# Optimization experiments

Hardware: AMD Instinct MI355X
Metric: run time of the kernel (lower is better)

The kernel has to match this reference:

```python
import jax, jax.numpy as jnp
import numpy as np

G = 8            # grid_size
G2 = G * G       # total_grid_size = 64
NS = 2.0         # neighborhood_size
H = 64           # h_dim
A = 1024         # bottleneck_dim == attention_dim
S = 32           # number of sequences
N = 64           # pedestrians per sequence
P = 4096         # scene boundary points per sequence (down_samples)
B = S * N        # total batch = 2048


def setup_inputs() -> dict:
    key = jax.random.key(0)
    ks = jax.random.split(key, 16)
    starts = jnp.arange(S, dtype=jnp.int32) * N
    seq_start_end = jnp.stack([starts, starts + N], axis=1)  # (S, 2) uniform groups
    return {
        "h_states": jax.random.normal(ks[0], (1, B, H), jnp.float32),
        "end_pos": jax.random.normal(ks[1], (B, 2), jnp.float32),
        "rel_pos": jax.random.normal(ks[2], (B, 2), jnp.float32) * 0.1,
        "scene_info": jax.random.normal(ks[3], (S, P, 2), jnp.float32),
        # Attention_Decoder params (soft attention over G2 grid cells, encoder_dim=1)
        "W_enc": jax.random.normal(ks[4], (1, A), jnp.float32) * 0.05,
        "b_enc": jnp.zeros((A,), jnp.float32),
        "W_dec": jax.random.normal(ks[5], (H, A), jnp.float32) * 0.05,
        "b_dec": jnp.zeros((A,), jnp.float32),
        "w_full": jax.random.normal(ks[6], (A, 1), jnp.float32) * 0.05,
        "b_full": jnp.zeros((1,), jnp.float32),
        "W_out": jax.random.normal(ks[7], (1 + H + 4, A), jnp.float32) * 0.05,  # [ctx, h, embed_info]
        "b_out": jnp.zeros((A,), jnp.float32),
        # mlp_pool: Linear(A, A) + BatchNorm1d + ReLU
        "W_mlp": jax.random.normal(ks[8], (A, A), jnp.float32) * 0.05,
        "b_mlp": jnp.zeros((A,), jnp.float32),
        "gamma": jnp.ones((A,), jnp.float32),
        "beta": jnp.zeros((A,), jnp.float32),
        "seq_start_end": seq_start_end,
    }


def _occupancy(end_pos, scene_info, num_seqs, peds, grid_size, ns):
    """Vectorized per-pedestrian grid-cell binning + scatter-add occupancy.
    end_pos: (num_seqs*peds, 2), scene_info: (num_seqs, P, 2) -> (B, G2)."""
    g2 = grid_size * grid_size
    b = num_seqs * peds
    ep = end_pos.reshape(num_seqs, peds, 1, 2)
    sx = scene_info[:, None, :, 0]  # (S, 1, P)
    sy = scene_info[:, None, :, 1]
    tl_x = ep[..., 0] - ns / 2
    tl_y = ep[..., 1] + ns / 2
    br_x = ep[..., 0] + ns / 2
    br_y = ep[..., 1] - ns / 2
    cell_x = jnp.floor((sx - tl_x) / ns * grid_size)   # (S, N, P)
    cell_y = jnp.floor((tl_y - sy) / ns * grid_size)
    cell = (cell_x + cell_y * grid_size).astype(jnp.int32)
    # point is out-of-bound if outside the ped's neighborhood box (matches torch mask)
    oob = (sx >= br_x) | (sx <= tl_x) | (sy >= tl_y) | (sy <= br_y)
    ped = jnp.arange(b, dtype=jnp.int32).reshape(num_seqs, peds, 1)
    # torch scatters masked points into slot 0 then drops it; we use one dump slot at the end
    idx = jnp.where(oob, b * g2, ped * g2 + cell)      # (S, N, P)
    counts = jax.ops.segment_sum(
        jnp.ones(idx.size, jnp.float32), idx.reshape(-1), num_segments=b * g2 + 1)
    return counts[:-1].reshape(b, g2)


def reference(h_states, end_pos, rel_pos, scene_info,
              W_enc, b_enc, W_dec, b_dec, w_full, b_full,
              W_out, b_out, W_mlp, b_mlp, gamma, beta, seq_start_end):
    num_seqs = seq_start_end.shape[0]
    b = end_pos.shape[0]
    peds = b // num_seqs
    occ = _occupancy(end_pos, scene_info, num_seqs, peds, G, NS)   # (B, G2)
    enc = occ[..., None]                                           # (B, G2, 1)
    h = h_states.reshape(b, -1)                                    # (B, H)
    embed_info = jnp.concatenate([end_pos, rel_pos], axis=1)       # (B, 4)
    # soft attention over the G2 grid cells conditioned on the decoder hidden state
    att = jax.nn.relu(enc @ W_enc + b_enc + (h @ W_dec + b_dec)[:, None, :])  # (B, G2, A)
    e = (att @ w_full)[..., 0] + b_full                            # (B, G2)
    alpha = jax.nn.softmax(e, axis=1)
    ctx = jnp.sum(alpha[..., None] * enc, axis=1)                  # (B, 1)
    pool = jnp.concatenate([ctx, h, embed_info], axis=1) @ W_out + b_out  # (B, A)
    # mlp_pool: Linear -> BatchNorm1d (training stats, biased var) -> ReLU
    y = pool @ W_mlp + b_mlp
    mu = jnp.mean(y, axis=0)
    var = jnp.mean((y - mu) ** 2, axis=0)
    y = gamma * (y - mu) * jax.lax.rsqrt(var + 1e-5) + beta
    return jax.nn.relu(y)
```

## Files before the change

kernel.cpp:

```cpp
#include <hip/hip_runtime.h>
#include <hip/hip_bf16.h>


#define NG2  64
#define NPTS 4096

typedef unsigned short ushort_t;
typedef __attribute__((ext_vector_type(8))) short bf16x8;
typedef __attribute__((ext_vector_type(4))) float f32x4;

struct PrepPtrs { const void* p[16]; };

__device__ __forceinline__ float bf2f(ushort_t u) {
  return __uint_as_float(((unsigned int)u) << 16);
}
__device__ __forceinline__ ushort_t f2bf(float f) {
  __hip_bfloat16 b = __float2bfloat16(f);
  return *reinterpret_cast<ushort_t*>(&b);
}
__device__ __forceinline__ float lde(const void* p, size_t i, int fl) {
  return fl ? bf2f(((const ushort_t*)p)[i]) : ((const float*)p)[i];
}
__device__ __forceinline__ int block_flag(const ushort_t* h) {
  __shared__ int bad_sh;
  if (threadIdx.x == 0) bad_sh = 0;
  __syncthreads();
  float v = bf2f(h[threadIdx.x & 255]);
  if (!(fabsf(v) <= 1e4f)) atomicOr(&bad_sh, 1);
  __syncthreads();
  return (bad_sh == 0) ? 1 : 0;
}

__device__ __forceinline__ void tp_body(const void* in, int fl, int job,
                                        int Kin, int Kpad, ushort_t* out) {
  __shared__ ushort_t t[32][40];
  int n0 = (job & 31) * 32, k0 = (job >> 5) * 32;
  int r = threadIdx.x >> 3, c4 = (threadIdx.x & 7) * 4;
  ushort4 v = make_ushort4(0, 0, 0, 0);
  if (k0 + r < Kin) {
    size_t off = (size_t)(k0 + r) * 1024 + n0 + c4;
    if (fl) {
      v = *(const ushort4*)((const ushort_t*)in + off);
    } else {
      float4 f = *(const float4*)((const float*)in + off);
      v = make_ushort4(f2bf(f.x), f2bf(f.y), f2bf(f.z), f2bf(f.w));
    }
  }
  *(ushort4*)(&t[r][c4]) = v;
  __syncthreads();
  int n = threadIdx.x >> 3, kk = (threadIdx.x & 7) * 4;
  ushort4 o = make_ushort4(t[kk][n], t[kk + 1][n], t[kk + 2][n], t[kk + 3][n]);
  *(ushort4*)(out + (size_t)(n0 + n) * Kpad + k0 + kk) = o;
}

__global__ __launch_bounds__(256) void k_prep(PrepPtrs ptrs,
                                              float* __restrict__ conv,
                                              ushort_t* __restrict__ hbf,
                                              ushort_t* __restrict__ WdecT,
                                              ushort_t* __restrict__ WoutT,
                                              ushort_t* __restrict__ WmlpT,
                                              ushort_t* __restrict__ Xcat0,
                                              float* __restrict__ occ,
                                              float* __restrict__ stats) {
  int b = blockIdx.x;
  int fl = block_flag((const ushort_t*)ptrs.p[0]);
  if (b < 9) {
    int idx = (b * 256 + threadIdx.x) * 4;
    int seg = idx >> 10, off = idx & 1023;
    float4 o;
    if (fl) {
      const unsigned int* src = (const unsigned int*)ptrs.p[7 + seg];
      uint2 u = *(const uint2*)(src + (off >> 1));
      o.x = __uint_as_float((u.x & 0xFFFFu) << 16);
      o.y = __uint_as_float(u.x & 0xFFFF0000u);
      o.z = __uint_as_float((u.y & 0xFFFFu) << 16);
      o.w = __uint_as_float(u.y & 0xFFFF0000u);
    } else {
      o = *(const float4*)((const float*)ptrs.p[7 + seg] + off);
    }
    *(float4*)(conv + idx) = o;
  } else if (b < 73) {
    int i = (b - 9) * 256 + threadIdx.x;
    if (fl) {
      ((uint4*)hbf)[i] = ((const uint4*)ptrs.p[0])[i];
    } else {
      float4 f0 = ((const float4*)ptrs.p[0])[2 * i];
      float4 f1 = ((const float4*)ptrs.p[0])[2 * i + 1];
      ((ushort4*)hbf)[2 * i]     = make_ushort4(f2bf(f0.x), f2bf(f0.y), f2bf(f0.z), f2bf(f0.w));
      ((ushort4*)hbf)[2 * i + 1] = make_ushort4(f2bf(f1.x), f2bf(f1.y), f2bf(f1.z), f2bf(f1.w));
    }
  } else if (b < 137) {
    tp_body(ptrs.p[1], fl, b - 73, 64, 64, WdecT);
  } else if (b < 233) {
    const void* wout1 = fl ? (const void*)((const ushort_t*)ptrs.p[2] + 1024)
                           : (const void*)((const float*)ptrs.p[2] + 1024);
    tp_body(wout1, fl, b - 137, 68, 96, WoutT);
  } else if (b < 489) {
    __shared__ ushort_t t64[64 * 68];
    int job = b - 233;
    int n0 = (job & 15) * 64, k0 = (job >> 4) * 64;
    const void* in = ptrs.p[3];
#pragma unroll
    for (int i = 0; i < 4; i++) {
      int chunk = threadIdx.x + i * 256;
      int r = chunk >> 4, c4 = (chunk & 15) * 4;
      ushort4 v;
      size_t off = (size_t)(k0 + r) * 1024 + n0 + c4;
      if (fl) {
        v = *(const ushort4*)((const ushort_t*)in + off);
      } else {
        float4 f = *(const float4*)((const float*)in + off);
        v = make_ushort4(f2bf(f.x), f2bf(f.y), f2bf(f.z), f2bf(f.w));
      }
      *(ushort4*)(&t64[r * 68 + c4]) = v;
    }
    __syncthreads();
#pragma unroll
    for (int i = 0; i < 4; i++) {
      int chunk = threadIdx.x + i * 256;
      int n = chunk >> 4, k4 = (chunk & 15) * 4;
      ushort4 o = make_ushort4(t64[(k4 + 0) * 68 + n], t64[(k4 + 1) * 68 + n],
                               t64[(k4 + 2) * 68 + n], t64[(k4 + 3) * 68 + n]);
      *(ushort4*)(WmlpT + (size_t)(n0 + n) * 1024 + k0 + k4) = o;
    }
  } else if (b < 681) {
    int flat = (b - 489) * 256 + threadIdx.x;
    int e4 = flat * 4;
    int r = e4 / 96, c = e4 - r * 96;
    ushort4 v = make_ushort4(0, 0, 0, 0);
    if (c < 64) {
      if (fl) v = *(const ushort4*)((const ushort_t*)ptrs.p[0] + r * 64 + c);
      else {
        float4 f = *(const float4*)((const float*)ptrs.p[0] + r * 64 + c);
        v = make_ushort4(f2bf(f.x), f2bf(f.y), f2bf(f.z), f2bf(f.w));
      }
    } else if (c == 64) {
      v.x = f2bf(lde(ptrs.p[4], 2 * r, fl));
      v.y = f2bf(lde(ptrs.p[4], 2 * r + 1, fl));
      v.z = f2bf(lde(ptrs.p[5], 2 * r, fl));
      v.w = f2bf(lde(ptrs.p[5], 2 * r + 1, fl));
    }
    *(ushort4*)(Xcat0 + e4) = v;
  } else if (b < 2729) {
    int i = b - 681;
    int s = i >> 6;
    __shared__ float cnth[NG2];
    if (threadIdx.x < NG2) cnth[threadIdx.x] = 0.0f;
    __syncthreads();
    float ex = lde(ptrs.p[4], 2 * i, fl), ey = lde(ptrs.p[4], 2 * i + 1, fl);
    float tlx = ex - 1.0f, tly = ey + 1.0f, brx = ex + 1.0f, bry = ey - 1.0f;
    const void* scn = ptrs.p[6];
    for (int p = threadIdx.x; p < NPTS; p += 256) {
      size_t pi = (size_t)s * NPTS + p;
      float sx, sy;
      if (fl) {
        unsigned int u = ((const unsigned int*)scn)[pi];
        sx = __uint_as_float((u & 0xFFFFu) << 16);
        sy = __uint_as_float(u & 0xFFFF0000u);
      } else {
        float2 f = *((const float2*)scn + pi);
        sx = f.x; sy = f.y;
      }
      bool oob = (sx >= brx) || (sx <= tlx) || (sy >= tly) || (sy <= bry);
      if (!oob) {
        int cx = (int)floorf((sx - tlx) * 0.5f * 8.0f);
        int cy = (int)floorf((tly - sy) * 0.5f * 8.0f);
        int cell = cx + cy * 8;
        if (cell >= 0 && cell < NG2) atomicAdd(&cnth[cell], 1.0f);
      }
    }
    __syncthreads();
    if (threadIdx.x < NG2) occ[i * NG2 + threadIdx.x] = cnth[threadIdx.x];
  } else {
#pragma unroll
    for (int k = 0; k < 8; k++) stats[threadIdx.x + 256 * k] = 0.0f;
  }
}

template <int K, int EPI>
__device__ __forceinline__ void mgemm_body(
    ushort_t* As, ushort_t* Bs, int m0, int n0,
    const ushort_t* __restrict__ A, int lda,
    const ushort_t* __restrict__ BT, int ldb,
    const float* __restrict__ bias1, const float* __restrict__ bias2,
    ushort_t* __restrict__ outb, float* __restrict__ outf) {
  int tid = threadIdx.x;
  int wave = tid >> 6, lane = tid & 63, l15 = lane & 15, kg = lane >> 4;
  f32x4 acc[4][2] = {};
  int ar = tid >> 2, ag = tid & 3;
  int aswz = ag ^ ((ar >> 1) & 3);
  for (int k0 = 0; k0 < K; k0 += 32) {
    uint4 av = *(const uint4*)(A + (size_t)(m0 + ar) * lda + k0 + ag * 8);
    *(uint4*)(&As[ar * 32 + aswz * 8]) = av;
#pragma unroll
    for (int i = 0; i < 2; i++) {
      int c = tid + i * 256;
      int br = c >> 2, bg = c & 3;
      int bswz = bg ^ ((br >> 1) & 3);
      uint4 bv = *(const uint4*)(BT + (size_t)(n0 + br) * ldb + k0 + bg * 8);
      *(uint4*)(&Bs[br * 32 + bswz * 8]) = bv;
    }
    __syncthreads();
    bf16x8 af[4], bfr[2];
#pragma unroll
    for (int mt = 0; mt < 4; mt++) {
      int row = mt * 16 + l15;
      int swz = kg ^ ((row >> 1) & 3);
      af[mt] = *(const bf16x8*)(&As[row * 32 + swz * 8]);
    }
#pragma unroll
    for (int nt = 0; nt < 2; nt++) {
      int row = wave * 32 + nt * 16 + l15;
      int swz = kg ^ ((row >> 1) & 3);
      bfr[nt] = *(const bf16x8*)(&Bs[row * 32 + swz * 8]);
    }
#pragma unroll
    for (int mt = 0; mt < 4; mt++)
#pragma unroll
      for (int nt = 0; nt < 2; nt++)
        acc[mt][nt] = __builtin_amdgcn_mfma_f32_16x16x32_bf16(af[mt], bfr[nt], acc[mt][nt], 0, 0, 0);
    __syncthreads();
  }
#pragma unroll
  for (int nt = 0; nt < 2; nt++) {
    int col = n0 + wave * 32 + nt * 16 + l15;
    float bsum = (EPI == 0) ? (bias1[col] + bias2[col]) : bias1[col];
#pragma unroll
    for (int mt = 0; mt < 4; mt++) {
#pragma unroll
      for (int r = 0; r < 4; r++) {
        int rowm = m0 + mt * 16 + kg * 4 + r;
        float v = acc[mt][nt][r] + bsum;
        if (EPI == 3) outf[(size_t)rowm * 1024 + col] = v;
        else outb[(size_t)rowm * 1024 + col] = f2bf(v);
      }
    }
  }
}

__global__ __launch_bounds__(256) void k_gemm2(
    const ushort_t* __restrict__ hbf, const ushort_t* __restrict__ WdecT,
    const float* __restrict__ benc, const float* __restrict__ bdec,
    ushort_t* __restrict__ hd_out,
    const ushort_t* __restrict__ Xcat0, const ushort_t* __restrict__ WoutT,
    const float* __restrict__ bout, float* __restrict__ P1) {
  __shared__ ushort_t As[64 * 32];
  __shared__ ushort_t Bs[128 * 32];
  int m0 = blockIdx.x * 64, n0 = blockIdx.y * 128;
  if (blockIdx.z == 0)
    mgemm_body<64, 0>(As, Bs, m0, n0, hbf, 64, WdecT, 64, benc, bdec, hd_out, nullptr);
  else
    mgemm_body<96, 3>(As, Bs, m0, n0, Xcat0, 96, WoutT, 96, bout, nullptr, nullptr, P1);
}

__global__ __launch_bounds__(256) void k_ygemm(
    const ushort_t* __restrict__ A, const ushort_t* __restrict__ BT,
    const float* __restrict__ bias1, ushort_t* __restrict__ outb,
    float* __restrict__ stats) {
  __shared__ ushort_t As[64 * 32];
  __shared__ ushort_t Bs[128 * 32];
  int m0 = blockIdx.x * 64, n0 = blockIdx.y * 128;
  int tid = threadIdx.x;
  int wave = tid >> 6, lane = tid & 63, l15 = lane & 15, kg = lane >> 4;
  f32x4 acc[4][2] = {};
  int ar = tid >> 2, ag = tid & 3;
  int aswz = ag ^ ((ar >> 1) & 3);
  for (int k0 = 0; k0 < 1024; k0 += 32) {
    uint4 av = *(const uint4*)(A + (size_t)(m0 + ar) * 1024 + k0 + ag * 8);
    *(uint4*)(&As[ar * 32 + aswz * 8]) = av;
#pragma unroll
    for (int i = 0; i < 2; i++) {
      int c = tid + i * 256;
      int br = c >> 2, bg = c & 3;
      int bswz = bg ^ ((br >> 1) & 3);
      uint4 bv = *(const uint4*)(BT + (size_t)(n0 + br) * 1024 + k0 + bg * 8);
      *(uint4*)(&Bs[br * 32 + bswz * 8]) = bv;
    }
    __syncthreads();
    bf16x8 af[4], bfr[2];
#pragma unroll
    for (int mt = 0; mt < 4; mt++) {
      int row = mt * 16 + l15;
      int swz = kg ^ ((row >> 1) & 3);
      af[mt] = *(const bf16x8*)(&As[row * 32 + swz * 8]);
    }
#pragma unroll
    for (int nt = 0; nt < 2; nt++) {
      int row = wave * 32 + nt * 16 + l15;
      int swz = kg ^ ((row >> 1) & 3);
      bfr[nt] = *(const bf16x8*)(&Bs[row * 32 + swz * 8]);
    }
#pragma unroll
    for (int mt = 0; mt < 4; mt++)
#pragma unroll
      for (int nt = 0; nt < 2; nt++)
        acc[mt][nt] = __builtin_amdgcn_mfma_f32_16x16x32_bf16(af[mt], bfr[nt], acc[mt][nt], 0, 0, 0);
    __syncthreads();
  }
#pragma unroll
  for (int nt = 0; nt < 2; nt++) {
    int col = n0 + wave * 32 + nt * 16 + l15;
    float bsum = bias1[col];
    float s1 = 0.0f, s2 = 0.0f;
#pragma unroll
    for (int mt = 0; mt < 4; mt++) {
#pragma unroll
      for (int r = 0; r < 4; r++) {
        int rowm = m0 + mt * 16 + kg * 4 + r;
        float v = acc[mt][nt][r] + bsum;
        outb[(size_t)rowm * 1024 + col] = f2bf(v);
        s1 += v; s2 = fmaf(v, v, s2);
      }
    }
    s1 += __shfl_down(s1, 16); s2 += __shfl_down(s2, 16);
    s1 += __shfl_down(s1, 32); s2 += __shfl_down(s2, 32);
    if (lane < 16) {
      atomicAdd(&stats[col], s1);
      atomicAdd(&stats[1024 + col], s2);
    }
  }
}

__global__ __launch_bounds__(256) void k_ectx(
    const float* __restrict__ occ,
    const float* __restrict__ Wenc, const float* __restrict__ wfull,
    const float* __restrict__ w0, const float* __restrict__ P1,
    const ushort_t* __restrict__ hd, ushort_t* __restrict__ pool) {
  __shared__ float we_sh[1024];
  __shared__ float wf_sh[1024];
  __shared__ float hd_sh[4][1024];
  __shared__ float occ_sh[4][64];
  int wave = threadIdx.x >> 6, lane = threadIdx.x & 63;
  int p = blockIdx.x * 4 + wave;
  {
    int t = threadIdx.x * 4;
    *(float4*)&we_sh[t] = *(const float4*)(Wenc + t);
    *(float4*)&wf_sh[t] = *(const float4*)(wfull + t);
  }
  occ_sh[wave][lane] = occ[p * 64 + lane];
  {
    const ushort_t* hrow = hd + (size_t)p * 1024;
#pragma unroll
    for (int j = 0; j < 4; j++) {
      int a = lane * 4 + j * 256;
      ushort4 v = *(const ushort4*)(hrow + a);
      hd_sh[wave][a + 0] = bf2f(v.x);
      hd_sh[wave][a + 1] = bf2f(v.y);
      hd_sh[wave][a + 2] = bf2f(v.z);
      hd_sh[wave][a + 3] = bf2f(v.w);
    }
  }
  __syncthreads();
  float c = occ_sh[wave][lane];
  float s0 = 0.0f, s1 = 0.0f, s2 = 0.0f, s3 = 0.0f;
#pragma unroll 4
  for (int a = 0; a < 1024; a += 4) {
    float4 we4 = *(const float4*)&we_sh[a];
    float4 hd4 = *(const float4*)&hd_sh[wave][a];
    float4 wf4 = *(const float4*)&wf_sh[a];
    s0 += fmaxf(fmaf(c, we4.x, hd4.x), 0.0f) * wf4.x;
    s1 += fmaxf(fmaf(c, we4.y, hd4.y), 0.0f) * wf4.y;
    s2 += fmaxf(fmaf(c, we4.z, hd4.z), 0.0f) * wf4.z;
    s3 += fmaxf(fmaf(c, we4.w, hd4.w), 0.0f) * wf4.w;
  }
  float e_mine = (s0 + s1) + (s2 + s3);
  float m = e_mine;
#pragma unroll
  for (int off = 32; off > 0; off >>= 1) m = fmaxf(m, __shfl_xor(m, off));
  float xe = __expf(e_mine - m);
  float den = xe;
#pragma unroll
  for (int off = 32; off > 0; off >>= 1) den += __shfl_xor(den, off);
  float cp = xe * c;
#pragma unroll
  for (int off = 32; off > 0; off >>= 1) cp += __shfl_xor(cp, off);
  float ctx = cp / den;
#pragma unroll
  for (int j = 0; j < 16; j++) {
    int a = lane + j * 64;
    pool[(size_t)p * 1024 + a] = f2bf(fmaf(ctx, w0[a], P1[(size_t)p * 1024 + a]));
  }
}

__global__ void k_norm(const ushort_t* __restrict__ y_mf,
                       const float* __restrict__ stats,
                       const float* __restrict__ gamma, const float* __restrict__ beta,
                       const ushort_t* __restrict__ hsrc, void* __restrict__ out) {
  int fl = block_flag(hsrc);
  int idx = (blockIdx.x * 256 + threadIdx.x) * 4;
  int col = idx & 1023;
  float vv[4];
#pragma unroll
  for (int j = 0; j < 4; j++) vv[j] = bf2f(y_mf[idx + j]);
  float4 s1 = *(const float4*)(stats + col);
  float4 s2 = *(const float4*)(stats + 1024 + col);
  float4 gm = *(const float4*)(gamma + col);
  float4 bt = *(const float4*)(beta + col);
  const float ib = 1.0f / 2048.0f;
  float m1[4] = {s1.x, s1.y, s1.z, s1.w};
  float m2[4] = {s2.x, s2.y, s2.z, s2.w};
  float gg[4] = {gm.x, gm.y, gm.z, gm.w};
  float bb[4] = {bt.x, bt.y, bt.z, bt.w};
  float o[4];
#pragma unroll
  for (int j = 0; j < 4; j++) {
    float mu = m1[j] * ib;
    float var = fmaf(-mu, mu, m2[j] * ib);
    o[j] = fmaxf(fmaf(gg[j] * (vv[j] - mu), rsqrtf(var + 1e-5f), bb[j]), 0.0f);
  }
  if (fl) {
    ushort4 ov = make_ushort4(f2bf(o[0]), f2bf(o[1]), f2bf(o[2]), f2bf(o[3]));
    *(ushort4*)((ushort_t*)out + idx) = ov;
  } else {
    *(float4*)((float*)out + idx) = make_float4(o[0], o[1], o[2], o[3]);
  }
}

extern "C" void kernel_launch(void* const* d_in, const int* in_sizes, int n_in,
                              void* d_out, int out_size, void* d_ws, size_t ws_size,
                              hipStream_t stream) {
  float* ws = (float*)d_ws;
  float* conv   = ws;
  float* c_Wenc = conv + 0;
  float* c_benc = conv + 1024;
  float* c_bdec = conv + 2048;
  float* c_wful = conv + 3072;
  float* c_bout = conv + 4096;
  float* c_bmlp = conv + 5120;
  float* c_gam  = conv + 6144;
  float* c_bet  = conv + 7168;
  float* c_w0   = conv + 8192;
  float* occ    = ws + 9216;
  float* stats  = ws + 140288;
  float* P1     = ws + 142336;
  ushort_t* u0    = (ushort_t*)(ws + 2239488);
  ushort_t* hbf   = u0;
  ushort_t* WdecT = u0 + 131072;
  ushort_t* WoutT = u0 + 196608;
  ushort_t* WmlpT = u0 + 294912;
  ushort_t* Xcat0 = u0 + 1343488;
  ushort_t* y_mf  = u0 + 1540096;
  ushort_t* hd_bf   = (ushort_t*)d_out;
  ushort_t* pool_mf = (ushort_t*)d_out;

  PrepPtrs ptrs;
  ptrs.p[0] = d_in[0];
  ptrs.p[1] = d_in[6];
  ptrs.p[2] = d_in[10];
  ptrs.p[3] = d_in[12];
  ptrs.p[4] = d_in[1];
  ptrs.p[5] = d_in[2];
  ptrs.p[6] = d_in[3];
  ptrs.p[7]  = d_in[4];
  ptrs.p[8]  = d_in[5];
  ptrs.p[9]  = d_in[7];
  ptrs.p[10] = d_in[8];
  ptrs.p[11] = d_in[11];
  ptrs.p[12] = d_in[13];
  ptrs.p[13] = d_in[14];
  ptrs.p[14] = d_in[15];
  ptrs.p[15] = d_in[10];

  k_prep<<<2730, 256, 0, stream>>>(ptrs, conv, hbf, WdecT, WoutT, WmlpT,
                                   Xcat0, occ, stats);

  k_gemm2<<<dim3(32, 8, 2), 256, 0, stream>>>(hbf, WdecT, c_benc, c_bdec, hd_bf,
                                              Xcat0, WoutT, c_bout, P1);

  k_ectx<<<512, 256, 0, stream>>>(occ, c_Wenc, c_wful, c_w0, P1, hd_bf, pool_mf);

  k_ygemm<<<dim3(32, 8), 256, 0, stream>>>(pool_mf, WmlpT, c_bmlp, y_mf, stats);

  k_norm<<<2048, 256, 0, stream>>>(y_mf, stats, c_gam, c_bet,
                                   (const ushort_t*)d_in[0], d_out);
}
```

Baseline: 156.4 us.

## Move occupancy and W_mlp transpose into the GEMM kernel to overlap work

Takes the occupancy binning blocks and the W_mlp transpose blocks out of the prep kernel and runs them inside the first GEMM launch as extra block ranges. The prep kernel shrinks to the small conversion and transpose jobs those GEMMs depend on. The scene-point scan and the large weight transpose then run alongside the tensor-core GEMMs instead of sitting on the critical path before them. Shared memory becomes a union buffer sized for the largest role. Because of that, the GEMM blocks may see lower occupancy or contend with the scan blocks.

After: 151.9 us. 1.03x faster.

```diff
diff --git a/kernel.cpp b/kernel.cpp
--- a/kernel.cpp
+++ b/kernel.cpp
@@ -58,9 +58,7 @@
                                               ushort_t* __restrict__ hbf,
                                               ushort_t* __restrict__ WdecT,
                                               ushort_t* __restrict__ WoutT,
-                                              ushort_t* __restrict__ WmlpT,
                                               ushort_t* __restrict__ Xcat0,
-                                              float* __restrict__ occ,
                                               float* __restrict__ stats) {
   int b = blockIdx.x;
   int fl = block_flag((const ushort_t*)ptrs.p[0]);
@@ -95,36 +93,8 @@
     const void* wout1 = fl ? (const void*)((const ushort_t*)ptrs.p[2] + 1024)
                            : (const void*)((const float*)ptrs.p[2] + 1024);
     tp_body(wout1, fl, b - 137, 68, 96, WoutT);
-  } else if (b < 489) {
-    __shared__ ushort_t t64[64 * 68];
-    int job = b - 233;
-    int n0 = (job & 15) * 64, k0 = (job >> 4) * 64;
-    const void* in = ptrs.p[3];
-#pragma unroll
-    for (int i = 0; i < 4; i++) {
-      int chunk = threadIdx.x + i * 256;
-      int r = chunk >> 4, c4 = (chunk & 15) * 4;
-      ushort4 v;
-      size_t off = (size_t)(k0 + r) * 1024 + n0 + c4;
-      if (fl) {
-        v = *(const ushort4*)((const ushort_t*)in + off);
-      } else {
-        float4 f = *(const float4*)((const float*)in + off);
-        v = make_ushort4(f2bf(f.x), f2bf(f.y), f2bf(f.z), f2bf(f.w));
-      }
-      *(ushort4*)(&t64[r * 68 + c4]) = v;
-    }
-    __syncthreads();
-#pragma unroll
-    for (int i = 0; i < 4; i++) {
-      int chunk = threadIdx.x + i * 256;
-      int n = chunk >> 4, k4 = (chunk & 15) * 4;
-      ushort4 o = make_ushort4(t64[(k4 + 0) * 68 + n], t64[(k4 + 1) * 68 + n],
-                               t64[(k4 + 2) * 68 + n], t64[(k4 + 3) * 68 + n]);
-      *(ushort4*)(WmlpT + (size_t)(n0 + n) * 1024 + k0 + k4) = o;
-    }
-  } else if (b < 681) {
-    int flat = (b - 489) * 256 + threadIdx.x;
+  } else if (b < 425) {
+    int flat = (b - 233) * 256 + threadIdx.x;
     int e4 = flat * 4;
     int r = e4 / 96, c = e4 - r * 96;
     ushort4 v = make_ushort4(0, 0, 0, 0);
@@ -141,36 +111,6 @@
       v.w = f2bf(lde(ptrs.p[5], 2 * r + 1, fl));
     }
     *(ushort4*)(Xcat0 + e4) = v;
-  } else if (b < 2729) {
-    int i = b - 681;
-    int s = i >> 6;
-    __shared__ float cnth[NG2];
-    if (threadIdx.x < NG2) cnth[threadIdx.x] = 0.0f;
-    __syncthreads();
-    float ex = lde(ptrs.p[4], 2 * i, fl), ey = lde(ptrs.p[4], 2 * i + 1, fl);
-    float tlx = ex - 1.0f, tly = ey + 1.0f, brx = ex + 1.0f, bry = ey - 1.0f;
-    const void* scn = ptrs.p[6];
-    for (int p = threadIdx.x; p < NPTS; p += 256) {
-      size_t pi = (size_t)s * NPTS + p;
-      float sx, sy;
-      if (fl) {
-        unsigned int u = ((const unsigned int*)scn)[pi];
-        sx = __uint_as_float((u & 0xFFFFu) << 16);
-        sy = __uint_as_float(u & 0xFFFF0000u);
-      } else {
-        float2 f = *((const float2*)scn + pi);
-        sx = f.x; sy = f.y;
-      }
-      bool oob = (sx >= brx) || (sx <= tlx) || (sy >= tly) || (sy <= bry);
-      if (!oob) {
-        int cx = (int)floorf((sx - tlx) * 0.5f * 8.0f);
-        int cy = (int)floorf((tly - sy) * 0.5f * 8.0f);
-        int cell = cx + cy * 8;
-        if (cell >= 0 && cell < NG2) atomicAdd(&cnth[cell], 1.0f);
-      }
-    }
-    __syncthreads();
-    if (threadIdx.x < NG2) occ[i * NG2 + threadIdx.x] = cnth[threadIdx.x];
   } else {
 #pragma unroll
     for (int k = 0; k < 8; k++) stats[threadIdx.x + 256 * k] = 0.0f;
@@ -238,19 +178,86 @@
   }
 }
 
-__global__ __launch_bounds__(256) void k_gemm2(
+__global__ __launch_bounds__(256) void k_fused(
+    PrepPtrs ptrs,
     const ushort_t* __restrict__ hbf, const ushort_t* __restrict__ WdecT,
     const float* __restrict__ benc, const float* __restrict__ bdec,
     ushort_t* __restrict__ hd_out,
     const ushort_t* __restrict__ Xcat0, const ushort_t* __restrict__ WoutT,
-    const float* __restrict__ bout, float* __restrict__ P1) {
-  __shared__ ushort_t As[64 * 32];
-  __shared__ ushort_t Bs[128 * 32];
-  int m0 = blockIdx.x * 64, n0 = blockIdx.y * 128;
-  if (blockIdx.z == 0)
-    mgemm_body<64, 0>(As, Bs, m0, n0, hbf, 64, WdecT, 64, benc, bdec, hd_out, nullptr);
-  else
-    mgemm_body<96, 3>(As, Bs, m0, n0, Xcat0, 96, WoutT, 96, bout, nullptr, nullptr, P1);
+    const float* __restrict__ bout, float* __restrict__ P1,
+    ushort_t* __restrict__ WmlpT, float* __restrict__ occ) {
+  __shared__ __align__(16) char smem_raw[12288];
+  int b = blockIdx.x;
+  if (b < 512) {
+    ushort_t* As = (ushort_t*)smem_raw;
+    ushort_t* Bs = (ushort_t*)(smem_raw + 4096);
+    int bb = b & 255;
+    int m0 = (bb & 31) * 64, n0 = ((bb >> 5) & 7) * 128;
+    if (b < 256)
+      mgemm_body<64, 0>(As, Bs, m0, n0, hbf, 64, WdecT, 64, benc, bdec, hd_out, nullptr);
+    else
+      mgemm_body<96, 3>(As, Bs, m0, n0, Xcat0, 96, WoutT, 96, bout, nullptr, nullptr, P1);
+  } else if (b < 2560) {
+    int fl = block_flag((const ushort_t*)ptrs.p[0]);
+    int i = b - 512;
+    int s = i >> 6;
+    float* cnth = (float*)smem_raw;
+    if (threadIdx.x < NG2) cnth[threadIdx.x] = 0.0f;
+    __syncthreads();
+    float ex = lde(ptrs.p[4], 2 * i, fl), ey = lde(ptrs.p[4], 2 * i + 1, fl);
+    float tlx = ex - 1.0f, tly = ey + 1.0f, brx = ex + 1.0f, bry = ey - 1.0f;
+    const void* scn = ptrs.p[6];
+    for (int p = threadIdx.x; p < NPTS; p += 256) {
+      size_t pi = (size_t)s * NPTS + p;
+      float sx, sy;
+      if (fl) {
+        unsigned int u = ((const unsigned int*)scn)[pi];
+        sx = __uint_as_float((u & 0xFFFFu) << 16);
+        sy = __uint_as_float(u & 0xFFFF0000u);
+      } else {
+        float2 f = *((const float2*)scn + pi);
+        sx = f.x; sy = f.y;
+      }
+      bool oob = (sx >= brx) || (sx <= tlx) || (sy >= tly) || (sy <= bry);
+      if (!oob) {
+        int cx = (int)floorf((sx - tlx) * 0.5f * 8.0f);
+        int cy = (int)floorf((tly - sy) * 0.5f * 8.0f);
+        int cell = cx + cy * 8;
+        if (cell >= 0 && cell < NG2) atomicAdd(&cnth[cell], 1.0f);
+      }
+    }
+    __syncthreads();
+    if (threadIdx.x < NG2) occ[(size_t)i * NG2 + threadIdx.x] = cnth[threadIdx.x];
+  } else {
+    int fl = block_flag((const ushort_t*)ptrs.p[0]);
+    ushort_t* t64 = (ushort_t*)smem_raw;
+    int job = b - 2560;
+    int n0 = (job & 15) * 64, k0 = (job >> 4) * 64;
+    const void* in = ptrs.p[3];
+#pragma unroll
+    for (int i = 0; i < 4; i++) {
+      int chunk = threadIdx.x + i * 256;
+      int r = chunk >> 4, c4 = (chunk & 15) * 4;
+      ushort4 v;
+      size_t off = (size_t)(k0 + r) * 1024 + n0 + c4;
+      if (fl) {
+        v = *(const ushort4*)((const ushort_t*)in + off);
+      } else {
+        float4 f = *(const float4*)((const float*)in + off);
+        v = make_ushort4(f2bf(f.x), f2bf(f.y), f2bf(f.z), f2bf(f.w));
+      }
+      *(ushort4*)(&t64[r * 68 + c4]) = v;
+    }
+    __syncthreads();
+#pragma unroll
+    for (int i = 0; i < 4; i++) {
+      int chunk = threadIdx.x + i * 256;
+      int n = chunk >> 4, k4 = (chunk & 15) * 4;
+      ushort4 o = make_ushort4(t64[(k4 + 0) * 68 + n], t64[(k4 + 1) * 68 + n],
+                               t64[(k4 + 2) * 68 + n], t64[(k4 + 3) * 68 + n]);
+      *(ushort4*)(WmlpT + (size_t)(n0 + n) * 1024 + k0 + k4) = o;
+    }
+  }
 }
 
 __global__ __launch_bounds__(256) void k_ygemm(
@@ -461,11 +468,10 @@
   ptrs.p[14] = d_in[15];
   ptrs.p[15] = d_in[10];
 
-  k_prep<<<2730, 256, 0, stream>>>(ptrs, conv, hbf, WdecT, WoutT, WmlpT,
-                                   Xcat0, occ, stats);
-
-  k_gemm2<<<dim3(32, 8, 2), 256, 0, stream>>>(hbf, WdecT, c_benc, c_bdec, hd_bf,
-                                              Xcat0, WoutT, c_bout, P1);
+  k_prep<<<426, 256, 0, stream>>>(ptrs, conv, hbf, WdecT, WoutT, Xcat0, stats);
+
+  k_fused<<<2816, 256, 0, stream>>>(ptrs, hbf, WdecT, c_benc, c_bdec, hd_bf,
+                                    Xcat0, WoutT, c_bout, P1, WmlpT, occ);
 
   k_ectx<<<512, 256, 0, stream>>>(occ, c_Wenc, c_wful, c_w0, P1, hd_bf, pool_mf);
 
```
